# Performance work log

Hardware: AMD Instinct MI355X
Metric: run time of the kernel (lower is better)

## Reference

```python
import jax, jax.numpy as jnp
import numpy as np

T, B, E, H, V, L = 128, 64, 1024, 1024, 10000, 2  # emb_size must equal hidden_size (see decode layer)


def setup_inputs() -> dict:
    key = jax.random.key(0)
    ks = jax.random.split(key, 8)
    s = 0.05
    return {
        "inputs": jax.random.randint(ks[0], (T, B), 0, V),
        "hidden": jnp.zeros((L, B, H), jnp.float32),
        "emb_table": jax.random.normal(ks[1], (V, E), jnp.float32) * s,
        "Ww": jax.random.normal(ks[2], (L, H, E), jnp.float32) * s,
        "Wb": jnp.zeros((L, H), jnp.float32),
        "Uw": jax.random.normal(ks[3], (L, H, H), jnp.float32) * s,
        "Ub": jnp.zeros((L, H), jnp.float32),
        "Fw": jax.random.normal(ks[4], (L, E, H), jnp.float32) * s,
        "Fb": jnp.zeros((L, E), jnp.float32),
        "Dw": jax.random.normal(ks[5], (V, H), jnp.float32) * s,
        "Db": jnp.zeros((V,), jnp.float32),
    }


def reference(inputs, hidden, emb_table, Ww, Wb, Uw, Ub, Fw, Fb, Dw, Db):
    # Dropout is treated as identity (eval mode) for a deterministic reference.
    emb = emb_table[inputs]                     # [T,B,E]

    # --- timestep 0: true recurrence from the provided initial hidden state ---
    x = emb[0]                                  # [B,E]
    h0 = []
    for l in range(L):
        h = jnp.tanh(x @ Ww[l].T + Wb[l] + hidden[l] @ Uw[l].T + Ub[l])  # [B,H]
        x = jnp.tanh(h @ Fw[l].T + Fb[l])                                # [B,E]
        h0.append(h)
    logits0 = x @ Dw.T + Db                     # [B,V]

    # --- timesteps 1..T-1: faithful to the source's indexing bug, the recurrent
    # input h_previous_ts[l] is ALWAYS the timestep-0 state, so all remaining
    # timesteps are independent and can be batched over time. ---
    x = emb[1:]                                 # [T-1,B,E]
    h_rest = []
    for l in range(L):
        aU = h0[l] @ Uw[l].T + Ub[l]            # [B,H], shared across t>=1
        h = jnp.tanh(jnp.einsum('tbe,he->tbh', x, Ww[l]) + Wb[l] + aU)   # [T-1,B,H]
        x = jnp.tanh(jnp.einsum('tbh,eh->tbe', h, Fw[l]) + Fb[l])        # [T-1,B,E]
        h_rest.append(h)
    logits_rest = jnp.einsum('tbe,ve->tbv', x, Dw) + Db  # [T-1,B,V]

    logits = jnp.concatenate([logits0[None], logits_rest], axis=0)        # [T,B,V]

    # Hidden-state list returned by source: [t0_l0, t0_l1, t1_l0, t1_l1, ...]
    h_all = jnp.concatenate(
        [jnp.stack(h0)[None],                               # [1,L,B,H]
         jnp.stack(h_rest).transpose(1, 0, 2, 3)], axis=0   # [T-1,L,B,H]
    ).reshape(T * L, B, H)
    return logits, h_all
```

## Files before the change

### kernel.cpp

```cpp
#include <hip/hip_runtime.h>
#include <hip/hip_bf16.h>
#include <cstdint>
#include <cstddef>

#define T_DIM 128
#define B_DIM 64
#define E_DIM 1024
#define H_DIM 1024
#define V_DIM 10000
#define L_DIM 2
#define VP2   10240
#define MROWS 8192
#define WN    2097152
#define WL    1048576

typedef __bf16 bf16_t;
typedef bf16_t bf16x8 __attribute__((ext_vector_type(8)));
typedef bf16_t bf16x4 __attribute__((ext_vector_type(4)));
typedef float  f32x4  __attribute__((ext_vector_type(4)));

__device__ __forceinline__ void g2l16(const void* g, void* l) {
  __builtin_amdgcn_global_load_lds((const __attribute__((address_space(1))) void*)g,
                                   (__attribute__((address_space(3))) void*)l,
                                   16, 0, 0);
}

__device__ __forceinline__ float fast_tanh(float v) {
  v = fminf(15.f, fmaxf(-15.f, v));
  float e = __expf(2.f * v);
  return (e - 1.f) / (e + 1.f);
}

template<int BK>
__global__ __launch_bounds__(256)
void gemm_bt(const bf16_t* __restrict__ A, const bf16_t* __restrict__ Bm, int K,
             const float* __restrict__ bias, int Nvalid,
             const float* __restrict__ Z, int do_tanh,
             bf16_t* __restrict__ outb, int outb_stride,
             float* __restrict__ outf, long stride_t, int stride_b, int Mvalid,
             int BNT, long abatch, long bbatch, long biasbatch, long obatch)
{
  __shared__ alignas(16) bf16_t lA[128 * BK];
  __shared__ alignas(16) bf16_t lB[128 * BK];
  const int tid  = threadIdx.x;
  const int wid  = tid >> 6;
  const int lane = tid & 63;

  int bm, bn;
  if (BNT > 0) {
    int g   = blockIdx.x;
    int SM  = (gridDim.x / BNT) >> 3;
    int xcd = g & 7;
    int q   = g >> 3;
    bm = xcd * SM + (q % SM);
    bn = q / SM;
  } else {
    bn = blockIdx.x;
    bm = 0;
    int batch = blockIdx.y;
    A    += (size_t)batch * abatch;
    Bm   += (size_t)batch * bbatch;
    bias += (size_t)batch * biasbatch;
    if (outf) outf += (size_t)batch * obatch;
  }

  f32x4 zero = {0.f, 0.f, 0.f, 0.f};
  f32x4 acc[4][4];
#pragma unroll
  for (int i = 0; i < 4; ++i)
#pragma unroll
    for (int j = 0; j < 4; ++j) acc[i][j] = zero;

  constexpr int CW    = BK / 8;
  constexpr int CALLS = (128 * BK / 8) / 256;
  const bf16_t* gA[CALLS];
  const bf16_t* gB[CALLS];
  int ldsoff[CALLS];
#pragma unroll
  for (int u = 0; u < CALLS; ++u) {
    int chunk = (u * 4 + wid) * 64 + lane;
    int row = chunk / CW, cc = chunk % CW;
    gA[u] = A  + (size_t)(bm * 128 + row) * K + cc * 8;
    gB[u] = Bm + (size_t)(bn * 128 + row) * K + cc * 8;
    ldsoff[u] = chunk * 16;
  }

  const int mrow = (wid >> 1) * 64;
  const int ncol = (wid & 1) * 64;
  const int fr = lane & 15;
  const int fq = (lane >> 4) * 16;
  char* lAb = (char*)lA;
  char* lBb = (char*)lB;

  for (int k0 = 0; k0 < K; k0 += BK) {
    __syncthreads();
#pragma unroll
    for (int u = 0; u < CALLS; ++u) g2l16(gA[u] + k0, lAb + ldsoff[u]);
#pragma unroll
    for (int u = 0; u < CALLS; ++u) g2l16(gB[u] + k0, lBb + ldsoff[u]);
    __syncthreads();

#pragma unroll
    for (int kk = 0; kk < BK / 32; ++kk) {
      bf16x8 af[4], bfv[4];
#pragma unroll
      for (int t = 0; t < 4; ++t) {
        af[t]  = *(const bf16x8*)(lAb + (mrow + t * 16 + fr) * (2 * BK) + kk * 64 + fq);
        bfv[t] = *(const bf16x8*)(lBb + (ncol + t * 16 + fr) * (2 * BK) + kk * 64 + fq);
      }
#pragma unroll
      for (int tm = 0; tm < 4; ++tm)
#pragma unroll
        for (int tn = 0; tn < 4; ++tn)
          acc[tm][tn] = __builtin_amdgcn_mfma_f32_16x16x32_bf16(af[tm], bfv[tn], acc[tm][tn], 0, 0, 0);
    }
  }

  const int rb = (lane >> 4) * 4;
  const int cb = lane & 15;
#pragma unroll
  for (int tm = 0; tm < 4; ++tm) {
#pragma unroll
    for (int tn = 0; tn < 4; ++tn) {
      const int col = bn * 128 + ncol + tn * 16 + cb;
      const float bv = (col < Nvalid) ? bias[col] : 0.f;
#pragma unroll
      for (int r = 0; r < 4; ++r) {
        const int row = bm * 128 + mrow + tm * 16 + rb + r;
        float v = acc[tm][tn][r] + bv;
        if (Z) {
          int zr = (row < 64) ? row : 64 + (row & 63);
          v += Z[zr * 1024 + col];
        }
        if (do_tanh) v = fast_tanh(v);
        if (outb) outb[(size_t)row * outb_stride + col] = (bf16_t)v;
        if (outf && row < Mvalid && col < Nvalid) {
          long o = (long)(row >> 6) * stride_t + (long)(row & 63) * stride_b + col;
          outf[o] = v;
        }
      }
    }
  }
}

__global__ void k_cvt3(const float* __restrict__ a, const float* __restrict__ b,
                       const float* __restrict__ c, bf16_t* __restrict__ da,
                       bf16_t* __restrict__ db, bf16_t* __restrict__ dc) {
  int i = blockIdx.x * 256 + threadIdx.x;
  int j = i << 2;
  int sel = j >> 21;
  int loc = j & (WN - 1);
  const float* s = (sel == 0) ? a : (sel == 1) ? b : c;
  bf16_t*      d = (sel == 0) ? da : (sel == 1) ? db : dc;
  f32x4 v = *(const f32x4*)(s + loc);
  bf16x4 o;
#pragma unroll
  for (int k = 0; k < 4; ++k) o[k] = (bf16_t)v[k];
  *(bf16x4*)(d + loc) = o;
}

__global__ void k_cvt_dw4(const float* __restrict__ s, bf16_t* __restrict__ d) {
  int i = blockIdx.x * 256 + threadIdx.x;
  int j = i << 2;
  int r = j >> 10, c = j & 1023;
  f32x4 v = {0.f, 0.f, 0.f, 0.f};
  if (r < V_DIM) v = *(const f32x4*)(s + (size_t)r * 1024 + c);
  bf16x4 o;
#pragma unroll
  for (int k = 0; k < 4; ++k) o[k] = (bf16_t)v[k];
  *(bf16x4*)(d + j) = o;
}

__global__ void k_gather4(const int* __restrict__ inp, const float* __restrict__ etab,
                          bf16_t* __restrict__ X) {
  int i = blockIdx.x * 256 + threadIdx.x;
  int j = i << 2;
  int r = j >> 10, e = j & 1023;
  int idx = inp[r];
  f32x4 v = *(const f32x4*)(etab + (size_t)idx * 1024 + e);
  bf16x4 o;
#pragma unroll
  for (int k = 0; k < 4; ++k) o[k] = (bf16_t)v[k];
  *(bf16x4*)(X + j) = o;
}

__global__ void k_cvt_hidden4(const float* __restrict__ hid, bf16_t* __restrict__ d) {
  int i = blockIdx.x * 256 + threadIdx.x;
  int j = i << 2;
  int l = j >> 17, r = (j >> 10) & 127, e = j & 1023;
  f32x4 v = {0.f, 0.f, 0.f, 0.f};
  if (r < B_DIM) v = *(const f32x4*)(hid + (size_t)(l * B_DIM + r) * 1024 + e);
  bf16x4 o;
#pragma unroll
  for (int k = 0; k < 4; ++k) o[k] = (bf16_t)v[k];
  *(bf16x4*)(d + j) = o;
}

extern "C" void kernel_launch(void* const* d_in, const int* in_sizes, int n_in,
                              void* d_out, int out_size, void* d_ws, size_t ws_size,
                              hipStream_t stream) {
  const int*   inp    = (const int*)  d_in[0];
  const float* hidden = (const float*)d_in[1];
  const float* etab   = (const float*)d_in[2];
  const float* Ww     = (const float*)d_in[3];
  const float* Wb     = (const float*)d_in[4];
  const float* Uw     = (const float*)d_in[5];
  const float* Ub     = (const float*)d_in[6];
  const float* Fw     = (const float*)d_in[7];
  const float* Fb     = (const float*)d_in[8];
  const float* Dw     = (const float*)d_in[9];
  const float* Db     = (const float*)d_in[10];
  float* out = (float*)d_out;

  char* p = (char*)d_ws;
  auto carve = [&](size_t n) { char* r = p; p += (n + 255) & ~(size_t)255; return r; };
  bf16_t* Wbf  = (bf16_t*)carve((size_t)WN * 2);
  bf16_t* Ubf  = (bf16_t*)carve((size_t)WN * 2);
  bf16_t* Fbf  = (bf16_t*)carve((size_t)WN * 2);
  bf16_t* Dbf  = (bf16_t*)carve((size_t)VP2 * 1024 * 2);
  bf16_t* Xc   = (bf16_t*)carve((size_t)MROWS * 1024 * 2);
  bf16_t* Hc   = (bf16_t*)carve((size_t)MROWS * 1024 * 2);
  bf16_t* hidb = (bf16_t*)carve((size_t)L_DIM * 128 * 1024 * 2);
  bf16_t* h0b  = (bf16_t*)carve((size_t)128 * 1024 * 2);
  float*  Zbuf = (float*) carve((size_t)2 * 128 * 1024 * 4);
  float*  Z0 = Zbuf, * Z1 = Zbuf + 131072;

  float* hall = out + (size_t)T_DIM * B_DIM * V_DIM;
  const long ST_H = (long)L_DIM * B_DIM * H_DIM;
  const long ST_V = (long)B_DIM * V_DIM;

  k_cvt3       <<<3 * WN / 4 / 256, 256, 0, stream>>>(Ww, Uw, Fw, Wbf, Ubf, Fbf);
  k_cvt_dw4    <<<VP2 * 1024 / 4 / 256, 256, 0, stream>>>(Dw, Dbf);
  k_gather4    <<<MROWS * 1024 / 4 / 256, 256, 0, stream>>>(inp, etab, Xc);
  k_cvt_hidden4<<<L_DIM * 128 * 1024 / 4 / 256, 256, 0, stream>>>(hidden, hidb);

  gemm_bt<64><<<dim3(8, 2), 256, 0, stream>>>(hidb, Ubf, 1024,
      Ub, 1024, nullptr, 0, nullptr, 0,
      Zbuf, 0L, 1024, 64,
      0, (long)128 * 1024, (long)WL, 1024L, 131072L);

  for (int l = 0; l < L_DIM; ++l) {
    float* Zl = l ? Z1 : Z0;
    gemm_bt<64><<<dim3(8, 1), 256, 0, stream>>>(Xc, Wbf + (size_t)l * WL, 1024,
        Wb + l * 1024, 1024, Zl, 1, h0b, 1024,
        nullptr, 0L, 0, 0, 0, 0, 0, 0, 0);
    gemm_bt<64><<<dim3(8, 1), 256, 0, stream>>>(h0b, Ubf + (size_t)l * WL, 1024,
        Ub + l * 1024, 1024, nullptr, 0, nullptr, 0,
        Zl + 64 * 1024, 0L, 1024, 64, 0, 0, 0, 0, 0);
    gemm_bt<32><<<dim3(64 * 8), 256, 0, stream>>>(Xc, Wbf + (size_t)l * WL, 1024,
        Wb + l * 1024, 1024, Zl, 1, Hc, 1024,
        hall + (size_t)l * B_DIM * H_DIM, ST_H, 1024, MROWS,
        8, 0, 0, 0, 0);
    gemm_bt<32><<<dim3(64 * 8), 256, 0, stream>>>(Hc, Fbf + (size_t)l * WL, 1024,
        Fb + l * 1024, 1024, nullptr, 1, Xc, 1024,
        nullptr, 0L, 0, 0, 8, 0, 0, 0, 0);
  }

  gemm_bt<32><<<dim3(64 * 80), 256, 0, stream>>>(Xc, Dbf, 1024,
      Db, V_DIM, nullptr, 0, nullptr, 0,
      out, ST_V, V_DIM, MROWS,
      80, 0, 0, 0, 0);

  (void)in_sizes; (void)n_in; (void)out_size; (void)ws_size;
}
```

Measured before the change: 1.081 ms.

## Use 256x256-tile triple-buffered MFMA GEMM for the decoder projection

Replaces the 128x128 generic GEMM for the final vocabulary projection with a dedicated 256x256 tile kernel using 512 threads. The kernel uses a three-stage LDS ring filled by direct global-to-LDS loads and padded rows to avoid bank conflicts. It interleaves loads with MFMA work, raises wave priority during MFMA, and swizzles blocks across XCDs. The aim is higher arithmetic intensity and better load/compute overlap on the largest GEMM. In exchange it uses more LDS and registers per block, and the Dw rows padded to 10240 must be valid memory.

```diff
diff --git a/kernel.cpp b/kernel.cpp
--- a/kernel.cpp
+++ b/kernel.cpp
@@ -29,6 +29,136 @@
   v = fminf(15.f, fmaxf(-15.f, v));
   float e = __expf(2.f * v);
   return (e - 1.f) / (e + 1.f);
+}
+
+__global__ __launch_bounds__(512, 2)
+void gemm256_bt(const bf16_t* __restrict__ A, const bf16_t* __restrict__ Bm, int K,
+                const float* __restrict__ bias, int Nvalid,
+                float* __restrict__ outf, long stride_t, int stride_b, int BNT)
+{
+  constexpr int RS  = 80;
+  constexpr int ASZ = 256 * RS;
+  constexpr int BUF = 2 * ASZ;
+  __shared__ alignas(16) char lds[3 * BUF];
+
+  const int tid  = threadIdx.x;
+  const int wid  = tid >> 6;
+  const int lane = tid & 63;
+  const int wr = wid >> 2;
+  const int wc = wid & 3;
+  const int fr = lane & 15;
+  const int fq = (lane >> 4) * 16;
+
+  int g   = blockIdx.x;
+  int SM  = (gridDim.x / BNT) >> 3;
+  int xcd = g & 7;
+  int q   = g >> 3;
+  int bm  = xcd * SM + (q % SM);
+  int bn  = q / SM;
+
+  const bf16_t* gsrc[5];
+  int loff[5];
+#pragma unroll
+  for (int u = 0; u < 5; ++u) {
+    int c   = u * 512 + tid;
+    int isB = (c >= 1280) ? 1 : 0;
+    int cl  = isB ? (c - 1280) : c;
+    int r = cl / 5, qq = cl % 5;
+    if (qq == 4) qq = 0;
+    const bf16_t* base = isB ? (Bm + (size_t)(bn * 256 + r) * K)
+                             : (A  + (size_t)(bm * 256 + r) * K);
+    gsrc[u] = base + qq * 8;
+    loff[u] = c * 16;
+  }
+
+  int aoff[8], boff[4];
+#pragma unroll
+  for (int i = 0; i < 8; ++i) aoff[i] = (wr * 128 + i * 16 + fr) * RS + fq;
+#pragma unroll
+  for (int i = 0; i < 4; ++i) boff[i] = ASZ + (wc * 64 + i * 16 + fr) * RS + fq;
+
+  f32x4 zero = {0.f, 0.f, 0.f, 0.f};
+  f32x4 acc[8][4];
+#pragma unroll
+  for (int i = 0; i < 8; ++i)
+#pragma unroll
+    for (int j = 0; j < 4; ++j) acc[i][j] = zero;
+
+  const int NT = K >> 5;
+
+#pragma unroll
+  for (int u = 0; u < 5; ++u) g2l16(gsrc[u],      lds + loff[u]);
+#pragma unroll
+  for (int u = 0; u < 5; ++u) g2l16(gsrc[u] + 32, lds + BUF + loff[u]);
+
+  for (int t = 0; t < NT; ++t) {
+    if (t < NT - 1) asm volatile("s_waitcnt vmcnt(5)" ::: "memory");
+    else            asm volatile("s_waitcnt vmcnt(0)" ::: "memory");
+    __builtin_amdgcn_sched_barrier(0);
+    __builtin_amdgcn_s_barrier();
+    asm volatile("" ::: "memory");
+    __builtin_amdgcn_sched_barrier(0);
+
+    char* cbuf = lds + (t % 3) * BUF;
+    char* sbuf = lds + ((t + 2) % 3) * BUF;
+    const int  k2 = (t + 2) << 5;
+    const bool st = (t + 2) < NT;
+
+    bf16x8 bfv[4], af[4];
+#pragma unroll
+    for (int i = 0; i < 4; ++i) bfv[i] = *(const bf16x8*)(cbuf + boff[i]);
+#pragma unroll
+    for (int i = 0; i < 4; ++i) af[i]  = *(const bf16x8*)(cbuf + aoff[i]);
+    if (st) {
+      g2l16(gsrc[0] + k2, sbuf + loff[0]);
+      g2l16(gsrc[1] + k2, sbuf + loff[1]);
+      g2l16(gsrc[2] + k2, sbuf + loff[2]);
+    }
+    asm volatile("s_waitcnt lgkmcnt(0)" ::: "memory");
+    __builtin_amdgcn_sched_barrier(0);
+    __builtin_amdgcn_s_setprio(1);
+#pragma unroll
+    for (int mi = 0; mi < 4; ++mi)
+#pragma unroll
+      for (int ni = 0; ni < 4; ++ni)
+        acc[mi][ni] = __builtin_amdgcn_mfma_f32_16x16x32_bf16(af[mi], bfv[ni], acc[mi][ni], 0, 0, 0);
+    __builtin_amdgcn_s_setprio(0);
+
+#pragma unroll
+    for (int i = 0; i < 4; ++i) af[i] = *(const bf16x8*)(cbuf + aoff[4 + i]);
+    if (st) {
+      g2l16(gsrc[3] + k2, sbuf + loff[3]);
+      g2l16(gsrc[4] + k2, sbuf + loff[4]);
+    }
+    asm volatile("s_waitcnt lgkmcnt(0)" ::: "memory");
+    __builtin_amdgcn_sched_barrier(0);
+    __builtin_amdgcn_s_setprio(1);
+#pragma unroll
+    for (int mi = 0; mi < 4; ++mi)
+#pragma unroll
+      for (int ni = 0; ni < 4; ++ni)
+        acc[4 + mi][ni] = __builtin_amdgcn_mfma_f32_16x16x32_bf16(af[mi], bfv[ni], acc[4 + mi][ni], 0, 0, 0);
+    __builtin_amdgcn_s_setprio(0);
+  }
+
+  const int rb  = (lane >> 4) * 4;
+  const int cb_ = lane & 15;
+#pragma unroll
+  for (int mi = 0; mi < 8; ++mi) {
+#pragma unroll
+    for (int ni = 0; ni < 4; ++ni) {
+      const int col = bn * 256 + wc * 64 + ni * 16 + cb_;
+      if (col < Nvalid) {
+        const float bv = bias[col];
+#pragma unroll
+        for (int r = 0; r < 4; ++r) {
+          const int row = bm * 256 + wr * 128 + mi * 16 + rb + r;
+          long o = (long)(row >> 6) * stride_t + (long)(row & 63) * stride_b + col;
+          outf[o] = acc[mi][ni][r] + bv;
+        }
+      }
+    }
+  }
 }
 
 template<int BK>
@@ -256,10 +386,8 @@
         nullptr, 0L, 0, 0, 8, 0, 0, 0, 0);
   }
 
-  gemm_bt<32><<<dim3(64 * 80), 256, 0, stream>>>(Xc, Dbf, 1024,
-      Db, V_DIM, nullptr, 0, nullptr, 0,
-      out, ST_V, V_DIM, MROWS,
-      80, 0, 0, 0, 0);
+  gemm256_bt<<<dim3(32 * 40), 512, 0, stream>>>(Xc, Dbf, 1024,
+      Db, V_DIM, out, ST_V, V_DIM, 40);
 
   (void)in_sizes; (void)n_in; (void)out_size; (void)ws_size;
 }
```

New measurement: 990.8 us. 1.09x faster.
